# Optimization experiments

Hardware: AMD Instinct MI355X
Metric: run time of the kernel (lower is better)

## Reference

```python
import jax, jax.numpy as jnp
import numpy as np

K = 2            # top-k experts
SCALING = 16.0 / 16.0  # alpha / r


def setup_inputs() -> dict:
    key = jax.random.key(0)
    ks = jax.random.split(key, 7)
    B, T, D, O, E, R = 2, 4096, 2048, 2048, 8, 16
    return {
        "x": jax.random.normal(ks[0], (B, T, D), dtype=jnp.float32),
        "W": jax.random.normal(ks[1], (O, D), dtype=jnp.float32) * (1.0 / np.sqrt(D)),
        "b": jax.random.normal(ks[2], (O,), dtype=jnp.float32) * 0.02,
        "lora_A": jax.random.normal(ks[3], (E, R, D), dtype=jnp.float32) * (1.0 / np.sqrt(D)),
        "lora_B": jax.random.normal(ks[4], (E, O, R), dtype=jnp.float32) * 0.02,
        "gate_w": jax.random.normal(ks[5], (E, D), dtype=jnp.float32) * 0.02,
        "gate_b": jax.random.normal(ks[6], (E,), dtype=jnp.float32) * 0.02,
    }


def reference(x, W, b, lora_A, lora_B, gate_w, gate_b):
    orig_shape = x.shape
    D = orig_shape[-1]
    O = W.shape[0]
    x_flat = x.reshape(-1, D)                                  # [N, D]

    base = x_flat @ W.T + b                                    # [N, O]

    logits = x_flat @ gate_w.T + gate_b                        # [N, E] (eval: no noise)
    topk_logits, topk_idx = jax.lax.top_k(logits, K)           # [N, K]
    gates = jax.nn.softmax(topk_logits, axis=-1)               # [N, K]

    xA = jnp.einsum('nd,erd->ner', x_flat, lora_A)             # [N, E, R]
    delta_all = jnp.einsum('ner,eor->neo', xA, lora_B)         # [N, E, O]

    delta_topk = jnp.take_along_axis(delta_all, topk_idx[:, :, None], axis=1)  # [N, K, O]
    lora_update = jnp.sum(delta_topk * gates[:, :, None], axis=1)              # [N, O]

    out = base + SCALING * lora_update
    return out.reshape(*orig_shape[:-1], O)
```

## Files before the change

kernel.cpp:

```cpp
#include <hip/hip_runtime.h>
#include <hip/hip_bf16.h>
#include <stdint.h>

#define N_ROWS 8192
#define DIM    2048
#define OUTD   2048
#define NEXP   8
#define RNK    16
#define ZCOLS  128
#define KAUG   2176

typedef unsigned short u16;
typedef float  f32x4  __attribute__((ext_vector_type(4)));
typedef __bf16 bf16x8 __attribute__((ext_vector_type(8)));

__device__ __forceinline__ u16 f2bf(float f) {
  unsigned u = __float_as_uint(f);
  return (u16)((u + 0x7fffu + ((u >> 16) & 1u)) >> 16);
}

#define GLOAD(SRC, DST) __builtin_amdgcn_global_load_lds( \
    (__attribute__((address_space(1))) void*)(SRC), \
    (__attribute__((address_space(3))) void*)(DST), 16, 0, 0)

__global__ __launch_bounds__(256) void k2a_lora(
    const float* __restrict__ lA, u16* __restrict__ ab)
{
  const int t  = threadIdx.x;
  const int ar = blockIdx.x;
  const float* src = lA + (size_t)ar * DIM;
  u16* dst = ab + (size_t)ar * DIM;
  #pragma unroll
  for (int i = 0; i < 2; ++i) {
    int c = t * 4 + i * 1024;
    float4 v = *(const float4*)(src + c);
    ushort4 s; s.x = f2bf(v.x); s.y = f2bf(v.y); s.z = f2bf(v.z); s.w = f2bf(v.w);
    *(ushort4*)(dst + c) = s;
  }
}

__global__ __launch_bounds__(256) void kfw_fused(
    const float* __restrict__ x, const float* __restrict__ gw,
    const float* __restrict__ gb, const u16* __restrict__ ab,
    u16* __restrict__ xaug,
    const float* __restrict__ W, const float* __restrict__ lB,
    u16* __restrict__ waug)
{
  const int t = threadIdx.x;

  if (blockIdx.x >= 512) {
    const int o = blockIdx.x - 512;
    const float* wr = W + (size_t)o * DIM;
    u16* dst = waug + (size_t)o * KAUG;
    #pragma unroll
    for (int i = 0; i < 2; ++i) {
      int c = t * 4 + i * 1024;
      float4 v = *(const float4*)(wr + c);
      ushort4 s; s.x = f2bf(v.x); s.y = f2bf(v.y); s.z = f2bf(v.z); s.w = f2bf(v.w);
      *(ushort4*)(dst + c) = s;
    }
    if (t < ZCOLS) {
      int e = t >> 4, r = t & 15;
      dst[DIM + t] = f2bf(lB[((size_t)e * OUTD + o) * RNK + r]);
    }
    return;
  }

  __shared__ __align__(16) u16 la[2][8192];
  __shared__ __align__(16) u16 xb[1024];
  __shared__ float4 gates[16];

  const int wave = t >> 6;
  const int lane = t & 63;
  const int r    = t >> 4;
  const int q    = t & 15;
  const size_t row0 = (size_t)blockIdx.x * 16;

  int   lrow[4], lsch[4];
  #pragma unroll
  for (int i = 0; i < 4; ++i) {
    const int g = t + i * 256;
    lrow[i] = g >> 3;
    lsch[i] = (g & 7) ^ (lrow[i] & 7);
  }

  auto stage_la = [&](int c, int h) {
    const int C0 = c * 64;
    #pragma unroll
    for (int i = 0; i < 4; ++i) {
      const char* src = (const char*)(ab + (size_t)lrow[i] * DIM + C0 + lsch[i] * 8);
      GLOAD(src, (char*)la[h] + (wave * 64 + i * 256) * 16);
    }
  };

  stage_la(0, 0);
  __builtin_amdgcn_sched_barrier(0);

  float4 xv, gwv[8];
  xv = *(const float4*)(x + (row0 + r) * DIM + q * 4);
  #pragma unroll
  for (int e = 0; e < NEXP; ++e)
    gwv[e] = *(const float4*)(gw + (size_t)e * DIM + q * 4);

  float ga[NEXP] = {};
  f32x4 acc[2] = {};
  const int nfA = 2 * wave, nfB = 2 * wave + 1;

  for (int c = 0; c < 32; ++c) {
    const int C0 = c * 64;
    if (c + 1 < 32) stage_la(c + 1, (c + 1) & 1);
    __builtin_amdgcn_sched_barrier(0);
    float4 xvn, gwvn[8];
    if (c + 1 < 32) {
      xvn = *(const float4*)(x + (row0 + r) * DIM + C0 + 64 + q * 4);
      #pragma unroll
      for (int e = 0; e < NEXP; ++e)
        gwvn[e] = *(const float4*)(gw + (size_t)e * DIM + C0 + 64 + q * 4);
    }
    __builtin_amdgcn_sched_barrier(0);
    ushort4 s; s.x = f2bf(xv.x); s.y = f2bf(xv.y); s.z = f2bf(xv.z); s.w = f2bf(xv.w);
    *(ushort4*)(xaug + (row0 + r) * KAUG + C0 + q * 4) = s;
    #pragma unroll
    for (int e = 0; e < NEXP; ++e)
      ga[e] += xv.x * gwv[e].x + xv.y * gwv[e].y + xv.z * gwv[e].z + xv.w * gwv[e].w;
    {
      const int ch = q >> 1;
      const int by = r * 128 + ((ch ^ (r & 7)) * 16) + (q & 1) * 8;
      *(ushort4*)((char*)xb + by) = s;
    }
    if (c + 1 < 32) asm volatile("s_waitcnt vmcnt(22) lgkmcnt(0)" ::: "memory");
    else            asm volatile("s_waitcnt vmcnt(0) lgkmcnt(0)" ::: "memory");
    __builtin_amdgcn_sched_barrier(0);
    __builtin_amdgcn_s_barrier();

    const char* lab = (const char*)la[c & 1];
    #pragma unroll
    for (int ks = 0; ks < 2; ++ks) {
      const int ra  = lane & 15;
      const int pa  = ((ks * 4 + (lane >> 4)) ^ (ra & 7)) * 16;
      bf16x8 avf = *(const bf16x8*)((char*)xb + ra * 128 + pa);
      const int rbA = (lane & 15) + 16 * nfA;
      const int rbB = (lane & 15) + 16 * nfB;
      bf16x8 bvA = *(const bf16x8*)(lab + rbA * 128 + (((ks * 4 + (lane >> 4)) ^ (rbA & 7)) * 16));
      bf16x8 bvB = *(const bf16x8*)(lab + rbB * 128 + (((ks * 4 + (lane >> 4)) ^ (rbB & 7)) * 16));
      acc[0] = __builtin_amdgcn_mfma_f32_16x16x32_bf16(avf, bvA, acc[0], 0, 0, 0);
      acc[1] = __builtin_amdgcn_mfma_f32_16x16x32_bf16(avf, bvB, acc[1], 0, 0, 0);
    }
    __builtin_amdgcn_s_barrier();
    __builtin_amdgcn_sched_barrier(0);
    xv = xvn;
    #pragma unroll
    for (int e = 0; e < NEXP; ++e) gwv[e] = gwvn[e];
  }

  #pragma unroll
  for (int e = 0; e < NEXP; ++e) {
    float v = ga[e];
    v += __shfl_xor(v, 1); v += __shfl_xor(v, 2);
    v += __shfl_xor(v, 4); v += __shfl_xor(v, 8);
    ga[e] = v + gb[e];
  }
  if (q == 0) {
    int e0 = 0; float m0 = ga[0];
    #pragma unroll
    for (int e = 1; e < NEXP; ++e) if (ga[e] > m0) { m0 = ga[e]; e0 = e; }
    int e1 = (e0 == 0) ? 1 : 0; float m1 = ga[e1];
    #pragma unroll
    for (int e = 0; e < NEXP; ++e) if (e != e0 && ga[e] > m1) { m1 = ga[e]; e1 = e; }
    float tt  = expf(m1 - m0);
    float inv = 1.f / (1.f + tt);
    float4 gg; gg.x = inv; gg.y = tt * inv;
    gg.z = __int_as_float(e0); gg.w = __int_as_float(e1);
    gates[r] = gg;
  }
  __syncthreads();

  #pragma unroll
  for (int nfl = 0; nfl < 2; ++nfl) {
    const int e = 2 * wave + nfl;
    const int n = e * 16 + (lane & 15);
    #pragma unroll
    for (int j = 0; j < 4; ++j) {
      const int m = (lane >> 4) * 4 + j;
      float4 gg = gates[m];
      const float g = (e == __float_as_int(gg.z)) ? gg.x
                    : ((e == __float_as_int(gg.w)) ? gg.y : 0.f);
      xaug[(row0 + m) * KAUG + DIM + n] = f2bf(acc[nfl][j] * g);
    }
  }
}

__global__ __launch_bounds__(512, 2) void gemm256_pipe(
    const u16* __restrict__ A, int lda,
    const u16* __restrict__ Bm, int ldb,
    int Ksz, int grid_n,
    float* __restrict__ outF, int ldo, const float* __restrict__ bias)
{
  __shared__ __align__(16) u16 smem[65536];

  const int tid  = threadIdx.x;
  const int wave = tid >> 6;
  const int lane = tid & 63;

  int bid = blockIdx.x;
  const int nwg = gridDim.x;
  if ((nwg & 7) == 0) {
    const int cpx = nwg >> 3;
    bid = (bid & 7) * cpx + (bid >> 3);
  }
  const int tm = bid / grid_n;
  const int tn = bid % grid_n;
  const size_t row0 = (size_t)tm * 256;
  const size_t col0 = (size_t)tn * 256;

  const int l3  = lane >> 3;
  const int sch = ((lane & 7) ^ l3) << 4;
  const char* aSrc = (const char*)(A  + (row0 + (size_t)(wave * 8 + l3)) * lda) + sch;
  const char* bSrc = (const char*)(Bm + (col0 + (size_t)(wave * 8 + l3)) * ldb) + sch;
  const size_t arst = (size_t)lda * 128;
  const size_t brst = (size_t)ldb * 128;
  char* ldsA = (char*)smem + wave * 1024;
  char* ldsB = (char*)smem + 65536 + wave * 1024;

  auto stage = [&](int tt) {
    const size_t ko = (size_t)tt * 128;
    const int    sb = (tt & 1) << 15;
    #pragma unroll
    for (int i = 0; i < 4; ++i)
      GLOAD(aSrc + ko + i * arst, ldsA + sb + i * 8192);
    #pragma unroll
    for (int i = 0; i < 4; ++i)
      GLOAD(bSrc + ko + i * brst, ldsB + sb + i * 8192);
  };

  const int wm = wave >> 2, wn = wave & 3;
  const int x0 = ((lane >> 4) ^ (lane & 7)) << 4;
  const int offA0 = wm * 16384 + (lane & 15) * 128 + x0;
  const int offB0 = wn * 8192  + (lane & 15) * 128 + x0;

  f32x4 acc[8][4] = {};

  const int nk = Ksz / 64;
  stage(0); stage(1);

  for (int t = 0; t < nk; ++t) {
    if (t + 1 < nk) asm volatile("s_waitcnt vmcnt(8)" ::: "memory");
    else            asm volatile("s_waitcnt vmcnt(0)" ::: "memory");
    __builtin_amdgcn_s_barrier();
    __builtin_amdgcn_sched_barrier(0);

    const char* sa = (const char*)smem + ((t & 1) << 15);
    const char* sb = (const char*)smem + 65536 + ((t & 1) << 15);

    bf16x8 av0[8], bv0[4], av1[8], bv1[4];
    #pragma unroll
    for (int mf = 0; mf < 8; ++mf) av0[mf] = *(const bf16x8*)(sa + offA0 + mf * 2048);
    #pragma unroll
    for (int nf = 0; nf < 4; ++nf) bv0[nf] = *(const bf16x8*)(sb + offB0 + nf * 2048);
    __builtin_amdgcn_s_setprio(1);
    #pragma unroll
    for (int mf = 0; mf < 8; ++mf)
      #pragma unroll
      for (int nf = 0; nf < 2; ++nf)
        acc[mf][nf] = __builtin_amdgcn_mfma_f32_16x16x32_bf16(
            av0[mf], bv0[nf], acc[mf][nf], 0, 0, 0);
    __builtin_amdgcn_s_setprio(0);
    #pragma unroll
    for (int mf = 0; mf < 8; ++mf) av1[mf] = *(const bf16x8*)(sa + (offA0 ^ 64) + mf * 2048);
    #pragma unroll
    for (int nf = 0; nf < 4; ++nf) bv1[nf] = *(const bf16x8*)(sb + (offB0 ^ 64) + nf * 2048);
    __builtin_amdgcn_s_setprio(1);
    #pragma unroll
    for (int mf = 0; mf < 8; ++mf)
      #pragma unroll
      for (int nf = 2; nf < 4; ++nf)
        acc[mf][nf] = __builtin_amdgcn_mfma_f32_16x16x32_bf16(
            av0[mf], bv0[nf], acc[mf][nf], 0, 0, 0);
    __builtin_amdgcn_s_setprio(0);
    asm volatile("s_waitcnt lgkmcnt(0)" ::: "memory");
    __builtin_amdgcn_s_barrier();
    __builtin_amdgcn_sched_barrier(0);
    if (t + 2 < nk) stage(t + 2);
    __builtin_amdgcn_s_setprio(1);
    #pragma unroll
    for (int mf = 0; mf < 8; ++mf)
      #pragma unroll
      for (int nf = 0; nf < 4; ++nf)
        acc[mf][nf] = __builtin_amdgcn_mfma_f32_16x16x32_bf16(
            av1[mf], bv1[nf], acc[mf][nf], 0, 0, 0);
    __builtin_amdgcn_s_setprio(0);
  }

  #pragma unroll
  for (int nf = 0; nf < 4; ++nf) {
    const size_t c = col0 + wn * 64 + nf * 16 + (lane & 15);
    const float bvv = bias[c];
    #pragma unroll
    for (int mf = 0; mf < 8; ++mf) {
      const size_t rb = row0 + wm * 128 + mf * 16 + ((lane >> 4) << 2);
      #pragma unroll
      for (int j = 0; j < 4; ++j)
        outF[(rb + j) * (size_t)ldo + c] = acc[mf][nf][j] + bvv;
    }
  }
}

extern "C" void kernel_launch(void* const* d_in, const int* in_sizes, int n_in,
                              void* d_out, int out_size, void* d_ws, size_t ws_size,
                              hipStream_t stream) {
  const float* x  = (const float*)d_in[0];
  const float* W  = (const float*)d_in[1];
  const float* b  = (const float*)d_in[2];
  const float* lA = (const float*)d_in[3];
  const float* lB = (const float*)d_in[4];
  const float* gw = (const float*)d_in[5];
  const float* gb = (const float*)d_in[6];
  float* out = (float*)d_out;

  u16* xaug = (u16*)d_ws;
  u16* waug = xaug + (size_t)N_ROWS * KAUG;
  u16* ab   = waug + (size_t)OUTD * KAUG;

  hipLaunchKernelGGL(k2a_lora, dim3(ZCOLS), dim3(256), 0, stream, lA, ab);
  hipLaunchKernelGGL(kfw_fused, dim3(512 + OUTD), dim3(256), 0, stream,
                     x, gw, gb, ab, xaug, W, lB, waug);
  hipLaunchKernelGGL(gemm256_pipe,
                     dim3((N_ROWS / 256) * (OUTD / 256)), dim3(512), 0, stream,
                     xaug, KAUG, waug, KAUG, KAUG, OUTD / 256,
                     out, OUTD, b);
}
```

Before: 116.8 us.

## Stage LoRA-A tiles through registers and double-buffer x to drop a barrier

Replaces the direct global-to-LDS async loads of the LoRA-A tile with register prefetch of the next chunk followed by explicit LDS stores. The x-tile LDS buffer is double-buffered so the trailing barrier per iteration can be removed, leaving one barrier per chunk. The hand-tuned vmcnt wait is replaced by only an lgkmcnt wait. This trades async DMA for extra VGPRs and LDS store instructions, which may lower occupancy.

```diff
diff --git a/kernel.cpp b/kernel.cpp
--- a/kernel.cpp
+++ b/kernel.cpp
@@ -67,7 +67,7 @@
   }
 
   __shared__ __align__(16) u16 la[2][8192];
-  __shared__ __align__(16) u16 xb[1024];
+  __shared__ __align__(16) u16 xb[2][1024];
   __shared__ float4 gates[16];
 
   const int wave = t >> 6;
@@ -76,7 +76,7 @@
   const int q    = t & 15;
   const size_t row0 = (size_t)blockIdx.x * 16;
 
-  int   lrow[4], lsch[4];
+  int lrow[4], lsch[4];
   #pragma unroll
   for (int i = 0; i < 4; ++i) {
     const int g = t + i * 256;
@@ -84,18 +84,14 @@
     lsch[i] = (g & 7) ^ (lrow[i] & 7);
   }
 
-  auto stage_la = [&](int c, int h) {
-    const int C0 = c * 64;
-    #pragma unroll
-    for (int i = 0; i < 4; ++i) {
-      const char* src = (const char*)(ab + (size_t)lrow[i] * DIM + C0 + lsch[i] * 8);
-      GLOAD(src, (char*)la[h] + (wave * 64 + i * 256) * 16);
-    }
+  auto lab_load = [&](int c, int i) -> uint4 {
+    return *(const uint4*)((const char*)(ab + (size_t)lrow[i] * DIM + c * 64)
+                           + lsch[i] * 16);
   };
 
-  stage_la(0, 0);
-  __builtin_amdgcn_sched_barrier(0);
-
+  uint4 lab[4];
+  #pragma unroll
+  for (int i = 0; i < 4; ++i) lab[i] = lab_load(0, i);
   float4 xv, gwv[8];
   xv = *(const float4*)(x + (row0 + r) * DIM + q * 4);
   #pragma unroll
@@ -108,16 +104,20 @@
 
   for (int c = 0; c < 32; ++c) {
     const int C0 = c * 64;
-    if (c + 1 < 32) stage_la(c + 1, (c + 1) & 1);
-    __builtin_amdgcn_sched_barrier(0);
-    float4 xvn, gwvn[8];
+    uint4 labn[4]; float4 xvn, gwvn[8];
     if (c + 1 < 32) {
+      #pragma unroll
+      for (int i = 0; i < 4; ++i) labn[i] = lab_load(c + 1, i);
       xvn = *(const float4*)(x + (row0 + r) * DIM + C0 + 64 + q * 4);
       #pragma unroll
       for (int e = 0; e < NEXP; ++e)
         gwvn[e] = *(const float4*)(gw + (size_t)e * DIM + C0 + 64 + q * 4);
     }
     __builtin_amdgcn_sched_barrier(0);
+
+    #pragma unroll
+    for (int i = 0; i < 4; ++i)
+      *(uint4*)((char*)la[c & 1] + (t + i * 256) * 16) = lab[i];
     ushort4 s; s.x = f2bf(xv.x); s.y = f2bf(xv.y); s.z = f2bf(xv.z); s.w = f2bf(xv.w);
     *(ushort4*)(xaug + (row0 + r) * KAUG + C0 + q * 4) = s;
     #pragma unroll
@@ -126,28 +126,30 @@
     {
       const int ch = q >> 1;
       const int by = r * 128 + ((ch ^ (r & 7)) * 16) + (q & 1) * 8;
-      *(ushort4*)((char*)xb + by) = s;
-    }
-    if (c + 1 < 32) asm volatile("s_waitcnt vmcnt(22) lgkmcnt(0)" ::: "memory");
-    else            asm volatile("s_waitcnt vmcnt(0) lgkmcnt(0)" ::: "memory");
+      *(ushort4*)((char*)xb[c & 1] + by) = s;
+    }
+
+    asm volatile("s_waitcnt lgkmcnt(0)" ::: "memory");
     __builtin_amdgcn_sched_barrier(0);
     __builtin_amdgcn_s_barrier();
 
-    const char* lab = (const char*)la[c & 1];
+    const char* laP = (const char*)la[c & 1];
+    const char* xbP = (const char*)xb[c & 1];
     #pragma unroll
     for (int ks = 0; ks < 2; ++ks) {
-      const int ra  = lane & 15;
-      const int pa  = ((ks * 4 + (lane >> 4)) ^ (ra & 7)) * 16;
-      bf16x8 avf = *(const bf16x8*)((char*)xb + ra * 128 + pa);
+      const int ra = lane & 15;
+      const int pa = ((ks * 4 + (lane >> 4)) ^ (ra & 7)) * 16;
+      bf16x8 avf = *(const bf16x8*)(xbP + ra * 128 + pa);
       const int rbA = (lane & 15) + 16 * nfA;
       const int rbB = (lane & 15) + 16 * nfB;
-      bf16x8 bvA = *(const bf16x8*)(lab + rbA * 128 + (((ks * 4 + (lane >> 4)) ^ (rbA & 7)) * 16));
-      bf16x8 bvB = *(const bf16x8*)(lab + rbB * 128 + (((ks * 4 + (lane >> 4)) ^ (rbB & 7)) * 16));
+      bf16x8 bvA = *(const bf16x8*)(laP + rbA * 128 + (((ks * 4 + (lane >> 4)) ^ (rbA & 7)) * 16));
+      bf16x8 bvB = *(const bf16x8*)(laP + rbB * 128 + (((ks * 4 + (lane >> 4)) ^ (rbB & 7)) * 16));
       acc[0] = __builtin_amdgcn_mfma_f32_16x16x32_bf16(avf, bvA, acc[0], 0, 0, 0);
       acc[1] = __builtin_amdgcn_mfma_f32_16x16x32_bf16(avf, bvB, acc[1], 0, 0, 0);
     }
-    __builtin_amdgcn_s_barrier();
-    __builtin_amdgcn_sched_barrier(0);
+
+    #pragma unroll
+    for (int i = 0; i < 4; ++i) lab[i] = labn[i];
     xv = xvn;
     #pragma unroll
     for (int e = 0; e < NEXP; ++e) gwv[e] = gwvn[e];
```

Result: no change. 117.3 us (+0.4%).
